# Performance work log

Measured on AMD Instinct MI355X. Metric: run time of the kernel, lower is better.

Reference implementation:

```python
import jax, jax.numpy as jnp
import numpy as np

N_NODES = 50000
N_EDGES = 25000
NNZ = 800000
IN_DIM = 256
OUT_DIM = 256


def setup_inputs() -> dict:
    key = jax.random.key(0)
    k1, k2, k3, k4, k5 = jax.random.split(key, 5)
    X = jax.random.normal(k1, (N_NODES, IN_DIM), dtype=jnp.float32)
    node_idx = jax.random.randint(k2, (NNZ,), 0, N_NODES, dtype=jnp.int64)
    edge_idx = jax.random.randint(k3, (NNZ,), 0, N_EDGES, dtype=jnp.int64)
    # Xavier-uniform-ish weight, zero bias (matches reset_parameters)
    limit = float(np.sqrt(6.0 / (IN_DIM + OUT_DIM)))
    W = jax.random.uniform(k4, (IN_DIM, OUT_DIM), dtype=jnp.float32, minval=-limit, maxval=limit)
    b = jnp.zeros((OUT_DIM,), dtype=jnp.float32)
    return {"X": X, "node_idx": node_idx, "edge_idx": edge_idx, "W": W, "b": b}


def reference(X, node_idx, edge_idx, W, b):
    # Y = X @ W + b  -- dense GEMM
    Y = X @ W + b  # [N, out_dim]

    ones = jnp.ones(node_idx.shape[0], dtype=Y.dtype)
    # D_v = rowsum(H)^-0.5 (inf -> 0); D_e = colsum(H)^-1 (inf -> 0)
    deg_v = jax.ops.segment_sum(ones, node_idx, num_segments=N_NODES)
    deg_e = jax.ops.segment_sum(ones, edge_idx, num_segments=N_EDGES)
    d_v = jnp.where(deg_v > 0, deg_v ** -0.5, 0.0)  # [N]
    d_e = jnp.where(deg_e > 0, 1.0 / deg_e, 0.0)    # [E]

    # step1 = H^T @ (D_v X): gather scaled node rows, scatter-add into edges
    Z = d_v[:, None] * Y                                   # [N, out_dim]
    step1 = jax.ops.segment_sum(Z[node_idx], edge_idx, num_segments=N_EDGES)  # [E, out_dim]
    # step2 = D_e @ step1
    step2 = d_e[:, None] * step1                           # [E, out_dim]
    # step3 = H @ step2: gather edge rows, scatter-add into nodes
    step3 = jax.ops.segment_sum(step2[edge_idx], node_idx, num_segments=N_NODES)  # [N, out_dim]
    # final = D_v @ step3
    return d_v[:, None] * step3
```

## Files before the change

kernel.cpp:

```cpp
#include <hip/hip_runtime.h>

#define N_NODES 50000
#define N_EDGES 25000
#define NNZ     800000
#define DIM     256

#define CAP_E 88
#define CAP_V 56

#define NBE 98
#define NBV 196
#define CE_COARSE 8800
#define CV_COARSE 4500
#define NNZ_PB 2048
#define P1_BLOCKS 391
#define GEMM_BLOCKS 782

#define B_A1   0
#define B_CE   0
#define B_CV   3449600
#define B_CSRE 12800000
#define B_CSRV 17200000
#define B_WT   22800000
#define B_CURV 22931072
#define B_CURE 23131072
#define B_CCUR 23331072
#define B_DV   23332248

typedef __attribute__((ext_vector_type(8))) short s8v;
typedef __attribute__((ext_vector_type(4))) float f4v;

__device__ __forceinline__ unsigned short f2bf(float f) {
    unsigned u = __float_as_uint(f);
    u = (u + 0x7FFFu + ((u >> 16) & 1u)) >> 16;
    return (unsigned short)u;
}
__device__ __forceinline__ float bf2f(unsigned short h) {
    return __uint_as_float(((unsigned)h) << 16);
}

__global__ __launch_bounds__(256) void k_wt(
        const float* __restrict__ W, unsigned short* __restrict__ WTb) {
    int t = blockIdx.x * 256 + threadIdx.x;
    int n = t >> 5;
    int k0 = (t & 31) * 8;
    unsigned short o[8];
#pragma unroll
    for (int j = 0; j < 8; ++j) o[j] = f2bf(W[(size_t)(k0 + j) * DIM + n]);
    *(s8v*)(WTb + (size_t)n * DIM + k0) = *(const s8v*)o;
}

__global__ __launch_bounds__(256) void k_bg(
        const float* __restrict__ X,
        const unsigned short* __restrict__ WT,
        const float* __restrict__ bias,
        unsigned short* __restrict__ Yb,
        const int* __restrict__ node_idx, const int* __restrict__ edge_idx,
        unsigned* __restrict__ ccurE, unsigned* __restrict__ ccurV,
        unsigned* __restrict__ coarseE, unsigned* __restrict__ coarseV) {
    __shared__ __align__(16) char smem[39424];
    const int tid = threadIdx.x;

    if (blockIdx.x < GEMM_BLOCKS) {
        unsigned short (*As)[264] = (unsigned short (*)[264])smem;
        const int wv   = tid >> 6;
        const int lane = tid & 63;
        const int quad = lane >> 4;
        const int l16  = lane & 15;
        const int r0   = blockIdx.x * 64;
        const int nb   = wv * 64;

#pragma unroll
        for (int it = 0; it < 16; ++it) {
            int i   = tid + it * 256;
            int row = i >> 6;
            int c4  = i & 63;
            int src = r0 + row;
            src = (src < N_NODES) ? src : (N_NODES - 1);
            float4 p = *(const float4*)(X + (size_t)src * DIM + c4 * 4);
            unsigned short o[4] = {f2bf(p.x), f2bf(p.y), f2bf(p.z), f2bf(p.w)};
            *(ushort4*)(&As[row][c4 * 4]) = *(const ushort4*)o;
        }
        __syncthreads();

        f4v acc[4][4];
#pragma unroll
        for (int mt = 0; mt < 4; ++mt)
#pragma unroll
            for (int nt = 0; nt < 4; ++nt) acc[mt][nt] = (f4v){0.f, 0.f, 0.f, 0.f};

        for (int k0 = 0; k0 < DIM; k0 += 32) {
            s8v a[4], b[4];
#pragma unroll
            for (int nt = 0; nt < 4; ++nt) {
                int n = nb + nt * 16 + l16;
                b[nt] = *(const s8v*)(WT + (size_t)n * DIM + k0 + quad * 8);
            }
#pragma unroll
            for (int mt = 0; mt < 4; ++mt)
                a[mt] = *(const s8v*)(&As[mt * 16 + l16][k0 + quad * 8]);
#pragma unroll
            for (int mt = 0; mt < 4; ++mt)
#pragma unroll
                for (int nt = 0; nt < 4; ++nt)
                    acc[mt][nt] = __builtin_amdgcn_mfma_f32_16x16x32_bf16(
                        a[mt], b[nt], acc[mt][nt], 0, 0, 0);
        }

        float bv[4];
#pragma unroll
        for (int nt = 0; nt < 4; ++nt) bv[nt] = bias[nb + nt * 16 + l16];

#pragma unroll
        for (int mt = 0; mt < 4; ++mt) {
#pragma unroll
            for (int reg = 0; reg < 4; ++reg) {
                int row = r0 + mt * 16 + quad * 4 + reg;
                if (row < N_NODES) {
#pragma unroll
                    for (int nt = 0; nt < 4; ++nt) {
                        Yb[(size_t)row * DIM + nb + nt * 16 + l16] =
                            f2bf(acc[mt][nt][reg] + bv[nt]);
                    }
                }
            }
        }
        return;
    }

    unsigned* histE = (unsigned*)smem;
    unsigned* histV = histE + NBE;
    unsigned* baseE = histV + NBV;
    unsigned* baseV = baseE + NBE;
    unsigned* offE  = baseV + NBV;
    unsigned* offV  = offE + NBE;
    unsigned* scanE = offV + NBV;
    unsigned* scanV = scanE + 256;
    unsigned* nn    = scanV + 256;
    unsigned* bufE  = nn + 2;
    unsigned* dstE  = bufE + NNZ_PB;
    unsigned* bufV  = dstE + NNZ_PB;
    unsigned* dstV  = bufV + NNZ_PB;

    const int pb  = blockIdx.x - GEMM_BLOCKS;
    const int base = pb * NNZ_PB;

    if (tid < NBE) histE[tid] = 0;
    if (tid < NBV) histV[tid] = 0;
    __syncthreads();

    int idx0 = base + tid * 4;
    int idx1 = base + 1024 + tid * 4;
    bool ok0 = idx0 < NNZ, ok1 = idx1 < NNZ;
    int4 v0 = ok0 ? *(const int4*)(node_idx + idx0) : (int4){0,0,0,0};
    int4 e0 = ok0 ? *(const int4*)(edge_idx + idx0) : (int4){0,0,0,0};
    int4 v1 = ok1 ? *(const int4*)(node_idx + idx1) : (int4){0,0,0,0};
    int4 e1 = ok1 ? *(const int4*)(edge_idx + idx1) : (int4){0,0,0,0};
    int vv[8] = {v0.x, v0.y, v0.z, v0.w, v1.x, v1.y, v1.z, v1.w};
    int ee[8] = {e0.x, e0.y, e0.z, e0.w, e1.x, e1.y, e1.z, e1.w};

    unsigned short locE[8], locV[8];
#pragma unroll
    for (int j = 0; j < 8; ++j) {
        bool ok = (j < 4) ? ok0 : ok1;
        if (ok) {
            locE[j] = (unsigned short)atomicAdd(&histE[ee[j] >> 8], 1u);
            locV[j] = (unsigned short)atomicAdd(&histV[vv[j] >> 8], 1u);
        }
    }
    __syncthreads();
    if (tid < NBE) baseE[tid] = atomicAdd(&ccurE[tid], histE[tid]);
    if (tid < NBV) baseV[tid] = atomicAdd(&ccurV[tid], histV[tid]);
    scanE[tid] = (tid < NBE) ? histE[tid] : 0u;
    scanV[tid] = (tid < NBV) ? histV[tid] : 0u;
    __syncthreads();
    for (int off = 1; off < 256; off <<= 1) {
        unsigned tE = (tid >= off) ? scanE[tid - off] : 0u;
        unsigned tV = (tid >= off) ? scanV[tid - off] : 0u;
        __syncthreads();
        scanE[tid] += tE;
        scanV[tid] += tV;
        __syncthreads();
    }
    if (tid < NBE) offE[tid] = scanE[tid] - histE[tid];
    if (tid < NBV) offV[tid] = scanV[tid] - histV[tid];
    if (tid == 0) { nn[0] = scanE[255]; nn[1] = scanV[255]; }
    __syncthreads();

#pragma unroll
    for (int j = 0; j < 8; ++j) {
        bool ok = (j < 4) ? ok0 : ok1;
        if (ok) {
            unsigned e = (unsigned)ee[j], v = (unsigned)vv[j];
            unsigned be = e >> 8, bv = v >> 8;
            unsigned se = offE[be] + locE[j];
            unsigned pe = baseE[be] + locE[j];
            bufE[se] = ((e & 255u) << 16) | v;
            dstE[se] = (pe < CE_COARSE) ? (be * CE_COARSE + pe) : 0xFFFFFFFFu;
            unsigned sv = offV[bv] + locV[j];
            unsigned pv = baseV[bv] + locV[j];
            bufV[sv] = ((v & 255u) << 16) | e;
            dstV[sv] = (pv < CV_COARSE) ? (bv * CV_COARSE + pv) : 0xFFFFFFFFu;
        }
    }
    __syncthreads();

    unsigned nE = nn[0], nV = nn[1];
    for (unsigned i = tid; i < nE; i += 256) {
        unsigned d = dstE[i];
        if (d != 0xFFFFFFFFu) coarseE[d] = bufE[i];
    }
    for (unsigned i = tid; i < nV; i += 256) {
        unsigned d = dstV[i];
        if (d != 0xFFFFFFFFu) coarseV[d] = bufV[i];
    }
}

__global__ __launch_bounds__(1024) void k_fine(
        const unsigned* __restrict__ coarseE, const unsigned* __restrict__ coarseV,
        const unsigned* __restrict__ ccurE, const unsigned* __restrict__ ccurV,
        unsigned short* __restrict__ csrE, unsigned short* __restrict__ csrV,
        unsigned* __restrict__ cur_e, unsigned* __restrict__ cur_v,
        float* __restrict__ dv) {
    __shared__ unsigned cnt[256];
    __shared__ __align__(16) unsigned short slots[256 * CAP_E];
    const int tid = threadIdx.x;
    if (tid < 256) cnt[tid] = 0;
    __syncthreads();

    if (blockIdx.x < NBE) {
        int b = blockIdx.x;
        unsigned n = ccurE[b]; n = n < CE_COARSE ? n : CE_COARSE;
        const unsigned* src = coarseE + (size_t)b * CE_COARSE;
        for (unsigned i = tid; i < n; i += 1024) {
            unsigned p = src[i];
            unsigned f = p >> 16, v = p & 0xFFFFu;
            unsigned pos = atomicAdd(&cnt[f], 1u);
            if (pos < CAP_E) slots[f * CAP_E + pos] = (unsigned short)v;
        }
        __syncthreads();
        if (tid < 256) {
            int e = b * 256 + tid;
            if (e < N_EDGES) cur_e[e] = cnt[tid];
        }
        int rows = N_EDGES - b * 256; rows = rows < 256 ? rows : 256;
        unsigned q4 = (unsigned)rows * (CAP_E / 2) / 4;
        uint4* dst = (uint4*)(csrE + (size_t)b * 256 * CAP_E);
        const uint4* s = (const uint4*)slots;
        for (unsigned i = tid; i < q4; i += 1024) dst[i] = s[i];
    } else {
        int b = blockIdx.x - NBE;
        unsigned n = ccurV[b]; n = n < CV_COARSE ? n : CV_COARSE;
        const unsigned* src = coarseV + (size_t)b * CV_COARSE;
        for (unsigned i = tid; i < n; i += 1024) {
            unsigned p = src[i];
            unsigned f = p >> 16, e = p & 0xFFFFu;
            unsigned pos = atomicAdd(&cnt[f], 1u);
            if (pos < CAP_V) slots[f * CAP_V + pos] = (unsigned short)e;
        }
        __syncthreads();
        if (tid < 256) {
            int v = b * 256 + tid;
            if (v < N_NODES) {
                unsigned c = cnt[tid];
                cur_v[v] = c;
                dv[v] = c ? __frsqrt_rn((float)c) : 0.0f;
            }
        }
        int rows = N_NODES - b * 256; rows = rows < 256 ? rows : 256;
        unsigned q4 = (unsigned)rows * (CAP_V / 2) / 4;
        uint4* dst = (uint4*)(csrV + (size_t)b * 256 * CAP_V);
        const uint4* s = (const uint4*)slots;
        for (unsigned i = tid; i < q4; i += 1024) dst[i] = s[i];
    }
}

__global__ __launch_bounds__(256) void k_gather_edges(
        const unsigned short* __restrict__ Yb,
        const unsigned short* __restrict__ csrE,
        const unsigned* __restrict__ cur_e,
        const float* __restrict__ dv,
        unsigned short* __restrict__ S2) {
    int w = (blockIdx.x * 256 + threadIdx.x) >> 6;
    int lane = threadIdx.x & 63;
    if (w >= N_EDGES) return;
    unsigned deg = cur_e[w];
    unsigned cnt = deg < CAP_E ? deg : CAP_E;
    float sc = deg ? 1.0f / (float)deg : 0.0f;
    const unsigned short* lst = csrE + (size_t)w * CAP_E;
    unsigned idp = (lane < CAP_E / 2) ? ((const unsigned*)lst)[lane] : 0u;
    const unsigned short* xb = Yb + (size_t)lane * 4;

    float ax = 0.f, ay = 0.f, az = 0.f, aw = 0.f;

#define EFETCH(J, X0, X1, X2, X3, S0, S1, S2_, S3)                         \
    {                                                                      \
        unsigned p0 = __shfl(idp, (int)((J) >> 1));                        \
        unsigned p1 = __shfl(idp, (int)((J) >> 1) + 1);                    \
        unsigned v0 = p0 & 0xFFFFu, v1 = p0 >> 16;                         \
        unsigned v2 = p1 & 0xFFFFu, v3 = p1 >> 16;                         \
        S0 = dv[v0]; S1 = dv[v1]; S2_ = dv[v2]; S3 = dv[v3];               \
        X0 = *(const ushort4*)(xb + ((size_t)v0 << 8));                    \
        X1 = *(const ushort4*)(xb + ((size_t)v1 << 8));                    \
        X2 = *(const ushort4*)(xb + ((size_t)v2 << 8));                    \
        X3 = *(const ushort4*)(xb + ((size_t)v3 << 8));                    \
    }
#define ECONS(X0, X1, X2, X3, S0, S1, S2_, S3)                             \
    {                                                                      \
        ax = fmaf(S0, bf2f(X0.x), ax); ay = fmaf(S0, bf2f(X0.y), ay);      \
        az = fmaf(S0, bf2f(X0.z), az); aw = fmaf(S0, bf2f(X0.w), aw);      \
        ax = fmaf(S1, bf2f(X1.x), ax); ay = fmaf(S1, bf2f(X1.y), ay);      \
        az = fmaf(S1, bf2f(X1.z), az); aw = fmaf(S1, bf2f(X1.w), aw);      \
        ax = fmaf(S2_, bf2f(X2.x), ax); ay = fmaf(S2_, bf2f(X2.y), ay);    \
        az = fmaf(S2_, bf2f(X2.z), az); aw = fmaf(S2_, bf2f(X2.w), aw);    \
        ax = fmaf(S3, bf2f(X3.x), ax); ay = fmaf(S3, bf2f(X3.y), ay);      \
        az = fmaf(S3, bf2f(X3.z), az); aw = fmaf(S3, bf2f(X3.w), aw);      \
    }

    unsigned quads = cnt >> 2;
    unsigned j = 0;
    if (quads) {
        ushort4 a0, a1, a2, a3, b0, b1, b2, b3;
        float r0, r1, r2, r3, t0, t1, t2, t3;
        EFETCH(0u, a0, a1, a2, a3, r0, r1, r2, r3);
        unsigned q = 1;
        for (; q + 1 < quads; q += 2) {
            EFETCH(4u * q,      b0, b1, b2, b3, t0, t1, t2, t3);
            ECONS(a0, a1, a2, a3, r0, r1, r2, r3);
            EFETCH(4u * q + 4u, a0, a1, a2, a3, r0, r1, r2, r3);
            ECONS(b0, b1, b2, b3, t0, t1, t2, t3);
        }
        if (q < quads) {
            EFETCH(4u * q, b0, b1, b2, b3, t0, t1, t2, t3);
            ECONS(a0, a1, a2, a3, r0, r1, r2, r3);
            ECONS(b0, b1, b2, b3, t0, t1, t2, t3);
        } else {
            ECONS(a0, a1, a2, a3, r0, r1, r2, r3);
        }
        j = quads << 2;
    }
    for (; j < cnt; ++j) {
        unsigned p = __shfl(idp, (int)(j >> 1));
        unsigned v = (j & 1) ? (p >> 16) : (p & 0xFFFFu);
        float s = dv[v];
        ushort4 x = *(const ushort4*)(xb + ((size_t)v << 8));
        ax = fmaf(s, bf2f(x.x), ax); ay = fmaf(s, bf2f(x.y), ay);
        az = fmaf(s, bf2f(x.z), az); aw = fmaf(s, bf2f(x.w), aw);
    }
#undef EFETCH
#undef ECONS

    ushort4 o = {f2bf(sc * ax), f2bf(sc * ay), f2bf(sc * az), f2bf(sc * aw)};
    *(ushort4*)(S2 + (size_t)w * DIM + lane * 4) = o;
}

__global__ __launch_bounds__(256) void k_gather_nodes(
        const unsigned short* __restrict__ S2,
        const unsigned short* __restrict__ csrV,
        const unsigned* __restrict__ cur_v,
        const float* __restrict__ dv,
        float* __restrict__ out) {
    int w = (blockIdx.x * 256 + threadIdx.x) >> 6;
    int lane = threadIdx.x & 63;
    if (w >= N_NODES) return;
    unsigned cnt = cur_v[w]; cnt = cnt < CAP_V ? cnt : CAP_V;
    const unsigned short* lst = csrV + (size_t)w * CAP_V;
    unsigned idp = (lane < CAP_V / 2) ? ((const unsigned*)lst)[lane] : 0u;
    const unsigned short* sb = S2 + (size_t)lane * 4;

    float ax = 0.f, ay = 0.f, az = 0.f, aw = 0.f;

#define NFETCH(J, X0, X1, X2, X3)                                          \
    {                                                                      \
        unsigned p0 = __shfl(idp, (int)((J) >> 1));                        \
        unsigned p1 = __shfl(idp, (int)((J) >> 1) + 1);                    \
        unsigned e0 = p0 & 0xFFFFu, e1 = p0 >> 16;                         \
        unsigned e2 = p1 & 0xFFFFu, e3 = p1 >> 16;                         \
        X0 = *(const ushort4*)(sb + ((size_t)e0 << 8));                    \
        X1 = *(const ushort4*)(sb + ((size_t)e1 << 8));                    \
        X2 = *(const ushort4*)(sb + ((size_t)e2 << 8));                    \
        X3 = *(const ushort4*)(sb + ((size_t)e3 << 8));                    \
    }
#define NCONS(X0, X1, X2, X3)                                              \
    {                                                                      \
        ax += (bf2f(X0.x) + bf2f(X1.x)) + (bf2f(X2.x) + bf2f(X3.x));       \
        ay += (bf2f(X0.y) + bf2f(X1.y)) + (bf2f(X2.y) + bf2f(X3.y));       \
        az += (bf2f(X0.z) + bf2f(X1.z)) + (bf2f(X2.z) + bf2f(X3.z));       \
        aw += (bf2f(X0.w) + bf2f(X1.w)) + (bf2f(X2.w) + bf2f(X3.w));       \
    }

    unsigned quads = cnt >> 2;
    unsigned j = 0;
    if (quads) {
        ushort4 a0, a1, a2, a3, b0, b1, b2, b3;
        NFETCH(0u, a0, a1, a2, a3);
        unsigned q = 1;
        for (; q + 1 < quads; q += 2) {
            NFETCH(4u * q,      b0, b1, b2, b3);
            NCONS(a0, a1, a2, a3);
            NFETCH(4u * q + 4u, a0, a1, a2, a3);
            NCONS(b0, b1, b2, b3);
        }
        if (q < quads) {
            NFETCH(4u * q, b0, b1, b2, b3);
            NCONS(a0, a1, a2, a3);
            NCONS(b0, b1, b2, b3);
        } else {
            NCONS(a0, a1, a2, a3);
        }
        j = quads << 2;
    }
    for (; j < cnt; ++j) {
        unsigned p = __shfl(idp, (int)(j >> 1));
        unsigned e = (j & 1) ? (p >> 16) : (p & 0xFFFFu);
        ushort4 x = *(const ushort4*)(sb + ((size_t)e << 8));
        ax += bf2f(x.x); ay += bf2f(x.y); az += bf2f(x.z); aw += bf2f(x.w);
    }
#undef NFETCH
#undef NCONS

    float s = dv[w];
    float4 o = {s * ax, s * ay, s * az, s * aw};
    *(float4*)(out + (size_t)w * DIM + lane * 4) = o;
}

extern "C" void kernel_launch(void* const* d_in, const int* in_sizes, int n_in,
                              void* d_out, int out_size, void* d_ws, size_t ws_size,
                              hipStream_t stream) {
    (void)in_sizes; (void)n_in; (void)out_size; (void)ws_size;
    const float* X        = (const float*)d_in[0];
    const int*   node_idx = (const int*)d_in[1];
    const int*   edge_idx = (const int*)d_in[2];
    const float* W        = (const float*)d_in[3];
    const float* bias     = (const float*)d_in[4];
    float* out = (float*)d_out;
    char*  ws  = (char*)d_ws;

    unsigned short* S2      = (unsigned short*)(ws + B_A1);
    unsigned*       coarseE = (unsigned*)(ws + B_CE);
    unsigned*       coarseV = (unsigned*)(ws + B_CV);
    unsigned short* csrE    = (unsigned short*)(ws + B_CSRE);
    unsigned short* csrV    = (unsigned short*)(ws + B_CSRV);
    unsigned short* WTb     = (unsigned short*)(ws + B_WT);
    unsigned*       cur_v   = (unsigned*)(ws + B_CURV);
    unsigned*       cur_e   = (unsigned*)(ws + B_CURE);
    unsigned*       ccurE   = (unsigned*)(ws + B_CCUR);
    unsigned*       ccurV   = ccurE + NBE;
    float*          dv      = (float*)(ws + B_DV);

    unsigned short* Yb = (unsigned short*)d_out;

    (void)hipMemsetAsync(ccurE, 0, (NBE + NBV) * sizeof(unsigned), stream);

    k_wt<<<32, 256, 0, stream>>>(W, WTb);
    k_bg<<<GEMM_BLOCKS + P1_BLOCKS, 256, 0, stream>>>(
        X, WTb, bias, Yb, node_idx, edge_idx, ccurE, ccurV, coarseE, coarseV);
    k_fine<<<NBE + NBV, 1024, 0, stream>>>(coarseE, coarseV, ccurE, ccurV,
                                           csrE, csrV, cur_e, cur_v, dv);
    k_gather_edges<<<(N_EDGES * 64 + 255) / 256, 256, 0, stream>>>(
        Yb, csrE, cur_e, dv, S2);
    k_gather_nodes<<<(N_NODES * 64 + 255) / 256, 256, 0, stream>>>(
        S2, csrV, cur_v, dv, out);
}
```

Measured before the change: 241.7 us.

## Defer node-side CSR build into edge-gather kernel to overlap with gather

The node-side fine bucketing (writing csrV slots) moves out of the mid kernel, which now only counts node degrees and computes dv. The csrV construction runs as the first 196 blocks of a fused kernel whose remaining blocks do the edge gather. The aim is to shorten the serial mid stage and let the CSR construction overlap with the bandwidth-bound edge gather. The cost is that the coarse node buffer is read twice, and the csrV blocks now use 256 threads instead of 1024.

```diff
diff --git a/kernel.cpp b/kernel.cpp
--- a/kernel.cpp
+++ b/kernel.cpp
@@ -15,6 +15,7 @@
 #define NNZ_PB 2048
 #define P1_BLOCKS 391
 #define GEMM_BLOCKS 782
+#define GE_BLOCKS 6250
 
 #define B_A1   0
 #define B_CE   0
@@ -216,10 +217,10 @@
     }
 }
 
-__global__ __launch_bounds__(1024) void k_fine(
+__global__ __launch_bounds__(1024) void k_mid2(
         const unsigned* __restrict__ coarseE, const unsigned* __restrict__ coarseV,
         const unsigned* __restrict__ ccurE, const unsigned* __restrict__ ccurV,
-        unsigned short* __restrict__ csrE, unsigned short* __restrict__ csrV,
+        unsigned short* __restrict__ csrE,
         unsigned* __restrict__ cur_e, unsigned* __restrict__ cur_v,
         float* __restrict__ dv) {
     __shared__ unsigned cnt[256];
@@ -253,10 +254,8 @@
         unsigned n = ccurV[b]; n = n < CV_COARSE ? n : CV_COARSE;
         const unsigned* src = coarseV + (size_t)b * CV_COARSE;
         for (unsigned i = tid; i < n; i += 1024) {
-            unsigned p = src[i];
-            unsigned f = p >> 16, e = p & 0xFFFFu;
-            unsigned pos = atomicAdd(&cnt[f], 1u);
-            if (pos < CAP_V) slots[f * CAP_V + pos] = (unsigned short)e;
+            unsigned f = src[i] >> 16;
+            atomicAdd(&cnt[f], 1u);
         }
         __syncthreads();
         if (tid < 256) {
@@ -267,25 +266,47 @@
                 dv[v] = c ? __frsqrt_rn((float)c) : 0.0f;
             }
         }
+    }
+}
+
+__global__ __launch_bounds__(256) void k_gev(
+        const unsigned short* __restrict__ Yb,
+        const unsigned short* __restrict__ csrE,
+        const unsigned* __restrict__ cur_e,
+        const float* __restrict__ dv,
+        unsigned short* __restrict__ S2,
+        const unsigned* __restrict__ coarseV, const unsigned* __restrict__ ccurV,
+        unsigned short* __restrict__ csrV) {
+    __shared__ unsigned cnt[256];
+    __shared__ __align__(16) unsigned short slots[256 * CAP_V];
+    const int tid = threadIdx.x;
+
+    if (blockIdx.x < NBV) {
+        int b = blockIdx.x;
+        cnt[tid] = 0;
+        __syncthreads();
+        unsigned n = ccurV[b]; n = n < CV_COARSE ? n : CV_COARSE;
+        const unsigned* src = coarseV + (size_t)b * CV_COARSE;
+        for (unsigned i = tid; i < n; i += 256) {
+            unsigned p = src[i];
+            unsigned f = p >> 16, e = p & 0xFFFFu;
+            unsigned pos = atomicAdd(&cnt[f], 1u);
+            if (pos < CAP_V) slots[f * CAP_V + pos] = (unsigned short)e;
+        }
+        __syncthreads();
         int rows = N_NODES - b * 256; rows = rows < 256 ? rows : 256;
         unsigned q4 = (unsigned)rows * (CAP_V / 2) / 4;
         uint4* dst = (uint4*)(csrV + (size_t)b * 256 * CAP_V);
         const uint4* s = (const uint4*)slots;
-        for (unsigned i = tid; i < q4; i += 1024) dst[i] = s[i];
-    }
-}
-
-__global__ __launch_bounds__(256) void k_gather_edges(
-        const unsigned short* __restrict__ Yb,
-        const unsigned short* __restrict__ csrE,
-        const unsigned* __restrict__ cur_e,
-        const float* __restrict__ dv,
-        unsigned short* __restrict__ S2) {
-    int w = (blockIdx.x * 256 + threadIdx.x) >> 6;
-    int lane = threadIdx.x & 63;
+        for (unsigned i = tid; i < q4; i += 256) dst[i] = s[i];
+        return;
+    }
+
+    int w = ((blockIdx.x - NBV) * 256 + tid) >> 6;
+    int lane = tid & 63;
     if (w >= N_EDGES) return;
     unsigned deg = cur_e[w];
-    unsigned cnt = deg < CAP_E ? deg : CAP_E;
+    unsigned cnte = deg < CAP_E ? deg : CAP_E;
     float sc = deg ? 1.0f / (float)deg : 0.0f;
     const unsigned short* lst = csrE + (size_t)w * CAP_E;
     unsigned idp = (lane < CAP_E / 2) ? ((const unsigned*)lst)[lane] : 0u;
@@ -317,7 +338,7 @@
         az = fmaf(S3, bf2f(X3.z), az); aw = fmaf(S3, bf2f(X3.w), aw);      \
     }
 
-    unsigned quads = cnt >> 2;
+    unsigned quads = cnte >> 2;
     unsigned j = 0;
     if (quads) {
         ushort4 a0, a1, a2, a3, b0, b1, b2, b3;
@@ -339,7 +360,7 @@
         }
         j = quads << 2;
     }
-    for (; j < cnt; ++j) {
+    for (; j < cnte; ++j) {
         unsigned p = __shfl(idp, (int)(j >> 1));
         unsigned v = (j & 1) ? (p >> 16) : (p & 0xFFFFu);
         float s = dv[v];
@@ -455,10 +476,10 @@
     k_wt<<<32, 256, 0, stream>>>(W, WTb);
     k_bg<<<GEMM_BLOCKS + P1_BLOCKS, 256, 0, stream>>>(
         X, WTb, bias, Yb, node_idx, edge_idx, ccurE, ccurV, coarseE, coarseV);
-    k_fine<<<NBE + NBV, 1024, 0, stream>>>(coarseE, coarseV, ccurE, ccurV,
-                                           csrE, csrV, cur_e, cur_v, dv);
-    k_gather_edges<<<(N_EDGES * 64 + 255) / 256, 256, 0, stream>>>(
-        Yb, csrE, cur_e, dv, S2);
+    k_mid2<<<NBE + NBV, 1024, 0, stream>>>(coarseE, coarseV, ccurE, ccurV,
+                                           csrE, cur_e, cur_v, dv);
+    k_gev<<<NBV + GE_BLOCKS, 256, 0, stream>>>(
+        Yb, csrE, cur_e, dv, S2, coarseV, ccurV, csrV);
     k_gather_nodes<<<(N_NODES * 64 + 255) / 256, 256, 0, stream>>>(
         S2, csrV, cur_v, dv, out);
 }
```

Result: no change. 245.2 us (+1.5%).
